# Performance work log

Measured on AMD Instinct MI355X. Metric: run time of the kernel, lower is better.

The kernel has to match this reference:

```python
import jax, jax.numpy as jnp
import numpy as np
from jax import lax

B, T = 256, 256
FD = (768, 74, 35)      # text, audio, vision input feature dims
HD = (128, 64, 64)      # LSTM hidden sizes
LEN = sum(HD)           # 256, fused feature dim
TW = 2                  # time_window
EXT = TW * LEN + 1      # 513, extended_dim
RANK = 24
OUT = 1


def setup_inputs() -> dict:
    key = jax.random.key(0)
    ks = iter(jax.random.split(key, 32))
    def n(shape, scale=0.05):
        return jax.random.normal(next(ks), shape, dtype=jnp.float32) * scale
    inp = {
        "text": n((B, T, FD[0]), 1.0),
        "audio": n((B, T, FD[1]), 1.0),
        "vision": n((B, T, FD[2]), 1.0),
    }
    # LSTM params per subnet: W_ih [4H, D], W_hh [4H, H], combined bias [4H]
    for tag, d, h in (("t", FD[0], HD[0]), ("a", FD[1], HD[1]), ("v", FD[2], HD[2])):
        inp[f"Wih_{tag}"] = n((4 * h, d))
        inp[f"Whh_{tag}"] = n((4 * h, h))
        inp[f"b_{tag}"] = n((4 * h,))
    inp["W1"] = n((RANK * OUT, LEN))
    inp["b1"] = n((RANK * OUT,))
    inp["W2"] = n((RANK * OUT, EXT))
    inp["b2"] = n((RANK * OUT,))
    inp["fw"] = n((1, RANK), 1.0)  # fusion_weights, xavier_normal-like
    return inp


def _lstm_seq(x, Wih, Whh, b):
    # x: [B, T, D] -> all hidden states [B, T, H]; torch gate order i,f,g,o
    Bn = x.shape[0]
    H = Whh.shape[1]
    h0 = jnp.zeros((Bn, H), x.dtype)
    def step(carry, xt):
        h, c = carry
        g = xt @ Wih.T + h @ Whh.T + b
        i, f, gg, o = jnp.split(g, 4, axis=-1)
        c = jax.nn.sigmoid(f) * c + jax.nn.sigmoid(i) * jnp.tanh(gg)
        h = jax.nn.sigmoid(o) * jnp.tanh(c)
        return (h, c), h
    _, hs = lax.scan(step, (h0, h0), jnp.swapaxes(x, 0, 1))
    return jnp.swapaxes(hs, 0, 1)


def reference(text, audio, vision,
              Wih_t, Whh_t, b_t, Wih_a, Whh_a, b_a, Wih_v, Whh_v, b_v,
              W1, b1, W2, b2, fw):
    # SubNets (dropout is identity in eval mode)
    audio_h = _lstm_seq(audio, Wih_a, Whh_a, b_a)
    video_h = _lstm_seq(vision, Wih_v, Whh_v, b_v)
    text_h = _lstm_seq(text, Wih_t, Whh_t, b_t)
    z = jnp.concatenate((audio_h, video_h, text_h), axis=2)  # [B, T, LEN]
    # time_extend with time_window=2: [ones, z[:, i], z[:, (i+1) % T]]
    ones = jnp.ones((z.shape[0], z.shape[1], 1), z.dtype)
    shifts = [jnp.roll(z, -j, axis=1) for j in range(TW)]
    z_ext = jnp.concatenate([ones] + shifts, axis=2)  # [B, T, EXT]
    # fusion loop over idx (stride=1 -> all T), vectorized as batched GEMM + mean
    a = jnp.einsum('btl,rl->btr', z, W1) + b1          # [B, T, RANK*OUT]
    bb = jnp.einsum('bte,re->btr', z_ext, W2) + b2     # [B, T, RANK*OUT]
    z_fusion = (a * bb).mean(axis=1)                   # sum_i/len(idx)
    z_fusion = z_fusion.reshape(-1, RANK, OUT)
    z_output = jnp.einsum('r,bro->bo', fw[0], z_fusion)
    output = z_output.reshape(-1, OUT)
    norm = jnp.sum(jnp.linalg.norm(z.reshape(z.shape[0], -1), axis=1)) / z.shape[0]
    return output, norm
```

## Files before the change

kernel.cpp:

```cpp
#include <hip/hip_runtime.h>
#include <math.h>


typedef unsigned short ushortT;
typedef short bf16x8 __attribute__((ext_vector_type(8)));
typedef float f32x4 __attribute__((ext_vector_type(4)));

__device__ __forceinline__ unsigned int f2bf(float f) {
  unsigned int u = __float_as_uint(f);
  u += 0x7FFFu + ((u >> 16) & 1u);
  return u >> 16;
}
__device__ __forceinline__ unsigned int pk2bf(float lo, float hi) {
  return f2bf(lo) | (f2bf(hi) << 16);
}
__device__ __forceinline__ float bf2f(ushortT u) {
  return __uint_as_float(((unsigned int)u) << 16);
}

template <int KP, int KIN>
__global__ __launch_bounds__(256) void pad_cvt_k(const float* __restrict__ src,
                                                 ushortT* __restrict__ dst, int total) {
  const int i = blockIdx.x * 256 + threadIdx.x;
  if (i >= total) return;
  if constexpr (KP == KIN) {
    dst[i] = (ushortT)f2bf(src[i]);
  } else {
    const int row = i / KP, c = i - row * KP;
    dst[i] = (c < KIN) ? (ushortT)f2bf(src[(size_t)row * KIN + c]) : (ushortT)0;
  }
}

#define SA2 40
__global__ __launch_bounds__(512) void gemm_text2_k(const float* __restrict__ X,
                                                    const ushortT* __restrict__ W16,
                                                    const float* __restrict__ bias,
                                                    ushortT* __restrict__ Y16) {
  const int K = 768, N = 512;
  __shared__ __align__(16) ushortT As[128 * SA2];
  __shared__ __align__(16) ushortT Bs[256 * SA2];
  const unsigned int lin = blockIdx.x;
  const int gb = (int)(lin >> 4), rb = (int)(lin & 15);
  const int m0 = (gb * 8 + (rb & 7)) * 128;
  const int n0 = (rb >> 3) * 256;
  const int tid = threadIdx.x;
  const int wave = tid >> 6, lane = tid & 63;
  const int wr = wave >> 2, wc = wave & 3;
  const int lm = lane & 15, lq = lane >> 4;
  const int arow = tid >> 2, aq = (tid & 3) * 8;
  const int brow = tid >> 1, bq = (tid & 1) * 16;

  const float*   Xp = X + (size_t)(m0 + arow) * K + aq;
  const ushortT* Wp = W16 + (size_t)(n0 + brow) * K + bq;
  uint4* As_w = (uint4*)&As[arow * SA2 + aq];
  uint4* Bs_w = (uint4*)&Bs[brow * SA2 + bq];

  f32x4 acc[4][4];
#pragma unroll
  for (int i = 0; i < 4; i++)
#pragma unroll
    for (int j = 0; j < 4; j++) acc[i][j] = (f32x4){0.f, 0.f, 0.f, 0.f};

  for (int k0 = 0; k0 < K; k0 += 32) {
    const float4 a0 = *(const float4*)(Xp + k0);
    const float4 a1 = *(const float4*)(Xp + k0 + 4);
    const uint4 b0v = *(const uint4*)(Wp + k0);
    const uint4 b1v = *(const uint4*)(Wp + k0 + 8);
    __syncthreads();
    uint4 ao;
    ao.x = pk2bf(a0.x, a0.y); ao.y = pk2bf(a0.z, a0.w);
    ao.z = pk2bf(a1.x, a1.y); ao.w = pk2bf(a1.z, a1.w);
    As_w[0] = ao;
    Bs_w[0] = b0v;
    Bs_w[1] = b1v;
    __syncthreads();
    bf16x8 af[4], bfv[4];
#pragma unroll
    for (int mt = 0; mt < 4; mt++)
      af[mt] = *(const bf16x8*)&As[(wr * 64 + mt * 16 + lm) * SA2 + lq * 8];
#pragma unroll
    for (int nt = 0; nt < 4; nt++)
      bfv[nt] = *(const bf16x8*)&Bs[(wc * 64 + nt * 16 + lm) * SA2 + lq * 8];
#pragma unroll
    for (int mt = 0; mt < 4; mt++)
#pragma unroll
      for (int nt = 0; nt < 4; nt++)
        acc[mt][nt] = __builtin_amdgcn_mfma_f32_16x16x32_bf16(af[mt], bfv[nt], acc[mt][nt], 0, 0, 0);
  }
  float biasv[4];
#pragma unroll
  for (int nt = 0; nt < 4; nt++) biasv[nt] = bias[n0 + wc * 64 + nt * 16 + lm];
#pragma unroll
  for (int mt = 0; mt < 4; mt++) {
#pragma unroll
    for (int nt = 0; nt < 4; nt++) {
      const int row0 = m0 + wr * 64 + mt * 16 + lq * 4;
      const int col = n0 + wc * 64 + nt * 16 + lm;
#pragma unroll
      for (int r = 0; r < 4; r++)
        Y16[(size_t)(row0 + r) * N + col] = (ushortT)f2bf(acc[mt][nt][r] + biasv[nt]);
    }
  }
}

template <int KP>
__global__ __launch_bounds__(256) void gemm_xp_k(const ushortT* __restrict__ A16,
                                                 const ushortT* __restrict__ B16,
                                                 const float* __restrict__ bias,
                                                 ushortT* __restrict__ Y16) {
  constexpr int SB = KP + 8;
  __shared__ __align__(16) ushortT As[128 * SB];
  __shared__ __align__(16) ushortT Bs[128 * SB];
  const int n0 = blockIdx.x * 128;
  const int m0 = blockIdx.y * 128;
  const int tid = threadIdx.x;
  const int srow = tid >> 1, shalf = tid & 1;
  const int wave = tid >> 6, lane = tid & 63;
  const int wr = wave >> 1, wc = wave & 1;
  const int lm = lane & 15, lq = lane >> 4;

  const uint4* ap = (const uint4*)(A16 + (size_t)(m0 + srow) * KP + shalf * (KP / 2));
  const uint4* bp = (const uint4*)(B16 + (size_t)(n0 + srow) * KP + shalf * (KP / 2));
  uint4* aw = (uint4*)&As[srow * SB + shalf * (KP / 2)];
  uint4* bw = (uint4*)&Bs[srow * SB + shalf * (KP / 2)];
#pragma unroll
  for (int i = 0; i < KP / 16; i++) { aw[i] = ap[i]; bw[i] = bp[i]; }
  __syncthreads();

  constexpr int KC = KP / 32;
  f32x4 acc[4][4];
#pragma unroll
  for (int i = 0; i < 4; i++)
#pragma unroll
    for (int j = 0; j < 4; j++) acc[i][j] = (f32x4){0.f, 0.f, 0.f, 0.f};
#pragma unroll
  for (int ks = 0; ks < KC; ks++) {
    bf16x8 af[4], bfv[4];
#pragma unroll
    for (int mt = 0; mt < 4; mt++)
      af[mt] = *(const bf16x8*)&As[(wr * 64 + mt * 16 + lm) * SB + ks * 32 + lq * 8];
#pragma unroll
    for (int nt = 0; nt < 4; nt++)
      bfv[nt] = *(const bf16x8*)&Bs[(wc * 64 + nt * 16 + lm) * SB + ks * 32 + lq * 8];
#pragma unroll
    for (int mt = 0; mt < 4; mt++)
#pragma unroll
      for (int nt = 0; nt < 4; nt++)
        acc[mt][nt] = __builtin_amdgcn_mfma_f32_16x16x32_bf16(af[mt], bfv[nt], acc[mt][nt], 0, 0, 0);
  }
  float biasv[4];
#pragma unroll
  for (int nt = 0; nt < 4; nt++) biasv[nt] = bias[n0 + wc * 64 + nt * 16 + lm];
#pragma unroll
  for (int mt = 0; mt < 4; mt++) {
#pragma unroll
    for (int nt = 0; nt < 4; nt++) {
      const int row0 = m0 + wr * 64 + mt * 16 + lq * 4;
      const int col = n0 + wc * 64 + nt * 16 + lm;
#pragma unroll
      for (int r = 0; r < 4; r++)
        Y16[(size_t)(row0 + r) * 256 + col] = (ushortT)f2bf(acc[mt][nt][r] + biasv[nt]);
    }
  }
}

__device__ __forceinline__ void bar_lgkm() {
  asm volatile("s_waitcnt lgkmcnt(0)" ::: "memory");
  __builtin_amdgcn_sched_barrier(0);
  __builtin_amdgcn_s_barrier();
  __builtin_amdgcn_sched_barrier(0);
}

template <int H, int COFF, int CW>
__device__ __forceinline__ void recur_impl3(const ushortT* __restrict__ xp,
                                            const ushortT* __restrict__ Whh,
                                            ushortT* __restrict__ z,
                                            int bblk, char* smem_) {
  constexpr int KC = H / 32;
  constexpr int C4H = 4 * H;
  constexpr int HP = H + 8;
  constexpr int XP = C4H + 8;
  constexpr int RING = 6;
  constexpr int NCH4 = C4H / 256;
  constexpr int CRB = H / 8;
  constexpr int FPT = (64 * CRB) / 512;
  ushortT* hbuf = (ushortT*)smem_;
  ushortT* xps = hbuf + RING * 16 * HP;
  const int tid = threadIdx.x;
  const int s = tid >> 6, lane = tid & 63;
  const int lm = lane & 15, lq = lane >> 4;
  const int b0 = bblk * 16;
  const int srow = tid >> 5, sch = tid & 31;
  const ushortT* xrowp = xp + (size_t)(b0 + srow) * 256 * C4H + sch * (C4H / 32);
  ushortT* xdst0 = &xps[srow * XP + sch * (C4H / 32)];

  bf16x8 bw[4][KC];
  if (s < CW) {
#pragma unroll
    for (int g = 0; g < 4; g++)
#pragma unroll
      for (int kc = 0; kc < KC; kc++) {
        const int n = g * H + s * 16 + lm;
        bw[g][kc] = *(const bf16x8*)(Whh + (size_t)n * H + kc * 32 + lq * 8);
      }
  }
  for (int i = tid; i < 16 * HP; i += 512) hbuf[(RING - 1) * 16 * HP + i] = 0;

  uint4 svA[NCH4], svB[NCH4];
  {
    const uint4* s0 = (const uint4*)(xrowp);
#pragma unroll
    for (int i = 0; i < NCH4; i++) svA[i] = s0[i];
    uint4* d0 = (uint4*)xdst0;
#pragma unroll
    for (int i = 0; i < NCH4; i++) d0[i] = svA[i];
    const uint4* s1 = (const uint4*)(xrowp + (size_t)C4H);
#pragma unroll
    for (int i = 0; i < NCH4; i++) svB[i] = s1[i];
  }
  float cst[4] = {0.f, 0.f, 0.f, 0.f};
  __syncthreads();

  auto step = [&](int t, uint4 (&svI)[NCH4], uint4 (&svC)[NCH4]) {
    if (t >= 4 && (t & 3) == 0) {
      const int t0 = t - 4;
#pragma unroll
      for (int i = 0; i < FPT; i++) {
        const int q = i * 512 + tid;
        const int m = q / (4 * CRB), j = (q / CRB) & 3, cr = q % CRB;
        const uint4 v = *(const uint4*)&hbuf[((t0 + j) % RING) * 16 * HP + m * HP + cr * 8];
        *(uint4*)&z[((size_t)(b0 + m) * 256 + t0 + j) * 256 + COFF + cr * 8] = v;
      }
    }
    {
      const int tn = (t + 2 < 256) ? t + 2 : 255;
      const uint4* src = (const uint4*)(xrowp + (size_t)tn * C4H);
#pragma unroll
      for (int i = 0; i < NCH4; i++) svI[i] = src[i];
    }
    {
      uint4* dst = (uint4*)(xdst0 + ((t + 1) & 1) * 16 * XP);
#pragma unroll
      for (int i = 0; i < NCH4; i++) dst[i] = svC[i];
    }
    if (s < CW) {
      const ushortT* hb = &hbuf[((t + RING - 1) % RING) * 16 * HP + lm * HP];
      bf16x8 af[KC];
#pragma unroll
      for (int kc = 0; kc < KC; kc++) af[kc] = *(const bf16x8*)(hb + kc * 32 + lq * 8);
      f32x4 acc[4];
#pragma unroll
      for (int g = 0; g < 4; g++) acc[g] = (f32x4){0.f, 0.f, 0.f, 0.f};
#pragma unroll
      for (int kc = 0; kc < KC; kc++)
#pragma unroll
        for (int g = 0; g < 4; g++)
          acc[g] = __builtin_amdgcn_mfma_f32_16x16x32_bf16(af[kc], bw[g][kc], acc[g], 0, 0, 0);
      const ushortT* xb = &xps[(t & 1) * 16 * XP];
      ushortT* hw = &hbuf[(t % RING) * 16 * HP];
      const int col = s * 16 + lm;
#pragma unroll
      for (int r = 0; r < 4; r++) {
        const int xrow = (lq * 4 + r) * XP;
        const float iv = acc[0][r] + bf2f(xb[xrow + 0 * H + col]);
        const float fv = acc[1][r] + bf2f(xb[xrow + 1 * H + col]);
        const float gg = acc[2][r] + bf2f(xb[xrow + 2 * H + col]);
        const float ov = acc[3][r] + bf2f(xb[xrow + 3 * H + col]);
        const float ei = __expf(-iv), ef = __expf(-fv), eg = __expf(-2.f * gg);
        const float pi = 1.f + ei, pf = 1.f + ef, pg = 1.f + eg;
        const float cc = (cst[r] * pi * pg + (1.f - eg) * pf) *
                         __builtin_amdgcn_rcpf(pf * pi * pg);
        cst[r] = cc;
        const float ec = __expf(-2.f * cc), eo = __expf(-ov);
        const float hv = (1.f - ec) * __builtin_amdgcn_rcpf((1.f + eo) * (1.f + ec));
        hw[(lq * 4 + r) * HP + col] = (ushortT)f2bf(hv);
      }
    }
    bar_lgkm();
  };

  for (int t = 0; t < 256; t += 2) {
    step(t, svA, svB);
    step(t + 1, svB, svA);
  }
  {
    const int t0 = 252;
#pragma unroll
    for (int i = 0; i < FPT; i++) {
      const int q = i * 512 + tid;
      const int m = q / (4 * CRB), j = (q / CRB) & 3, cr = q % CRB;
      const uint4 v = *(const uint4*)&hbuf[((t0 + j) % RING) * 16 * HP + m * HP + cr * 8];
      *(uint4*)&z[((size_t)(b0 + m) * 256 + t0 + j) * 256 + COFF + cr * 8] = v;
    }
  }
}

__global__ __launch_bounds__(512, 1) void recur3_k(const ushortT* __restrict__ xpt,
                                                   const ushortT* __restrict__ xpa,
                                                   const ushortT* __restrict__ xpv_,
                                                   const ushortT* __restrict__ Wt,
                                                   const ushortT* __restrict__ Wa,
                                                   const ushortT* __restrict__ Wv,
                                                   ushortT* __restrict__ z) {
  extern __shared__ char smem[];
  const int bid = blockIdx.x;
  if (bid < 16) recur_impl3<128, 128, 8>(xpt, Wt, z, bid, smem);
  else if (bid < 32) recur_impl3<64, 0, 4>(xpa, Wa, z, bid - 16, smem);
  else recur_impl3<64, 64, 4>(xpv_, Wv, z, bid - 32, smem);
}

__global__ __launch_bounds__(192) void fusion_k(const ushortT* __restrict__ z,
                                                const float* __restrict__ W1,
                                                const float* __restrict__ b1,
                                                const float* __restrict__ W2,
                                                const float* __restrict__ b2,
                                                const float* __restrict__ fw,
                                                float* __restrict__ s_acc,
                                                float* __restrict__ sumsq) {
  __shared__ __align__(16) float zs[256 * 36];
  __shared__ float red[8];
  const int tid = threadIdx.x;
  const int b = blockIdx.x >> 3;
  const int t0 = (blockIdx.x & 7) * 32;
  const ushortT* zb = z + (size_t)b * 65536;
  float sq = 0.0f;
  for (int idx = tid; idx < 33 * 256; idx += 192) {
    const int row = idx >> 8, k = idx & 255;
    int t = t0 + row; if (t >= 256) t -= 256;
    const float v = bf2f(zb[t * 256 + k]);
    zs[k * 36 + row] = v;
    if (row < 32) sq += v * v;
  }
  __syncthreads();
  const int dg = tid >> 3;
  const int rg = tid & 7;
  const float* w1p = W1 + dg * 256;
  const float* w2p = W2 + dg * 513;
  float aa[4] = {}, ab1[4] = {}, ab2[4] = {};
#pragma unroll 4
  for (int k = 0; k < 256; k++) {
    const float w1v = w1p[k];
    const float w21 = w2p[1 + k];
    const float w22 = w2p[257 + k];
    const float* zr = &zs[k * 36 + (rg << 2)];
    const float4 za = *(const float4*)zr;
    const float z4 = zr[4];
    aa[0]  += za.x * w1v; aa[1]  += za.y * w1v; aa[2]  += za.z * w1v; aa[3]  += za.w * w1v;
    ab1[0] += za.x * w21; ab1[1] += za.y * w21; ab1[2] += za.z * w21; ab1[3] += za.w * w21;
    ab2[0] += za.y * w22; ab2[1] += za.z * w22; ab2[2] += za.w * w22; ab2[3] += z4   * w22;
  }
  const float b1v = b1[dg];
  const float b2v = b2[dg] + w2p[0];
  const float fwv = fw[dg];
  float s = 0.0f;
#pragma unroll
  for (int i = 0; i < 4; i++) {
    const float a  = aa[i] + b1v;
    const float bb = ab1[i] + ab2[i] + b2v;
    s += a * bb;
  }
  s *= fwv;
#pragma unroll
  for (int off = 32; off > 0; off >>= 1) {
    s  += __shfl_down(s, off);
    sq += __shfl_down(sq, off);
  }
  const int wid = tid >> 6;
  if ((tid & 63) == 0) { red[wid * 2] = s; red[wid * 2 + 1] = sq; }
  __syncthreads();
  if (tid == 0) {
    atomicAdd(&s_acc[b], red[0] + red[2] + red[4]);
    atomicAdd(&sumsq[b], red[1] + red[3] + red[5]);
  }
}

__global__ __launch_bounds__(256) void final_k(const float* __restrict__ s_acc,
                                               const float* __restrict__ sumsq,
                                               float* __restrict__ out) {
  __shared__ float red[4];
  const int tid = threadIdx.x;
  out[tid] = s_acc[tid] * (1.0f / 256.0f);
  float sq = sqrtf(sumsq[tid]);
#pragma unroll
  for (int off = 32; off > 0; off >>= 1) sq += __shfl_down(sq, off);
  if ((tid & 63) == 0) red[tid >> 6] = sq;
  __syncthreads();
  if (tid == 0) out[256] = (red[0] + red[1] + red[2] + red[3]) * (1.0f / 256.0f);
}

extern "C" void kernel_launch(void* const* d_in, const int* in_sizes, int n_in,
                              void* d_out, int out_size, void* d_ws, size_t ws_size,
                              hipStream_t stream) {
  const float* text   = (const float*)d_in[0];
  const float* audio  = (const float*)d_in[1];
  const float* vision = (const float*)d_in[2];
  const float* Wih_t  = (const float*)d_in[3];
  const float* Whh_t  = (const float*)d_in[4];
  const float* b_t    = (const float*)d_in[5];
  const float* Wih_a  = (const float*)d_in[6];
  const float* Whh_a  = (const float*)d_in[7];
  const float* b_a    = (const float*)d_in[8];
  const float* Wih_v  = (const float*)d_in[9];
  const float* Whh_v  = (const float*)d_in[10];
  const float* b_v    = (const float*)d_in[11];
  const float* W1     = (const float*)d_in[12];
  const float* b1     = (const float*)d_in[13];
  const float* W2     = (const float*)d_in[14];
  const float* b2     = (const float*)d_in[15];
  const float* fw     = (const float*)d_in[16];

  ushortT* xpt = (ushortT*)d_ws;
  ushortT* xpa = xpt + (size_t)33554432;
  ushortT* xpv = xpa + (size_t)16777216;
  ushortT* z16 = xpv + (size_t)16777216;
  float* s_acc = (float*)(z16 + (size_t)16777216);
  float* sumsq = s_acc + 256;
  ushortT* WhhT16 = (ushortT*)(sumsq + 256);
  ushortT* WhhA16 = WhhT16 + 65536;
  ushortT* WhhV16 = WhhA16 + 16384;
  ushortT* A16a  = z16;
  ushortT* A16v  = A16a + (size_t)6291456;
  ushortT* Wt768 = A16v + (size_t)4194304;
  ushortT* WA16  = Wt768 + 393216;
  ushortT* WV16  = WA16 + 24576;

  hipMemsetAsync(s_acc, 0, 512 * sizeof(float), stream);

  pad_cvt_k<768, 768><<<1536, 256, 0, stream>>>(Wih_t, Wt768, 512 * 768);
  pad_cvt_k<128, 128><<<256, 256, 0, stream>>>(Whh_t, WhhT16, 512 * 128);
  pad_cvt_k<64, 64><<<64, 256, 0, stream>>>(Whh_a, WhhA16, 256 * 64);
  pad_cvt_k<64, 64><<<64, 256, 0, stream>>>(Whh_v, WhhV16, 256 * 64);
  pad_cvt_k<96, 74><<<96, 256, 0, stream>>>(Wih_a, WA16, 256 * 96);
  pad_cvt_k<64, 35><<<64, 256, 0, stream>>>(Wih_v, WV16, 256 * 64);
  pad_cvt_k<96, 74><<<24576, 256, 0, stream>>>(audio, A16a, 65536 * 96);
  pad_cvt_k<64, 35><<<16384, 256, 0, stream>>>(vision, A16v, 65536 * 64);

  gemm_text2_k<<<1024, 512, 0, stream>>>(text, Wt768, b_t, xpt);
  gemm_xp_k<96><<<dim3(2, 512), 256, 0, stream>>>(A16a, WA16, b_a, xpa);
  gemm_xp_k<64><<<dim3(2, 512), 256, 0, stream>>>(A16v, WV16, b_v, xpv);
  recur3_k<<<48, 512, 59392, stream>>>(xpt, xpa, xpv, WhhT16, WhhA16, WhhV16, z16);
  fusion_k<<<2048, 192, 0, stream>>>(z16, W1, b1, W2, b2, fw, s_acc, sumsq);
  final_k<<<1, 256, 0, stream>>>(s_acc, sumsq, (float*)d_out);
}
```

Measured before the change: 925.4 us.

## Store input projections in per-lane fragment layout so recurrence reads them directly

The input-projection GEMM epilogues now scatter results into a layout ordered by block, timestep and MFMA fragment position. In that layout each compute lane of the recurrence kernel can fetch its gate inputs for a step with two contiguous 16-byte global loads. This drops the previous path that staged projections through shared memory, along with its staging copies and the extra LDS reads per step, and it reduces the dynamic shared memory size. The price is scattered, strided 2-byte global stores in the GEMM epilogues, and the recurrence now depends on global-load latency being hidden by a two-step prefetch.

New measurement: 846.5 us. 8.5% less time.

```diff
diff --git a/kernel.cpp b/kernel.cpp
--- a/kernel.cpp
+++ b/kernel.cpp
@@ -36,7 +36,7 @@
                                                     const ushortT* __restrict__ W16,
                                                     const float* __restrict__ bias,
                                                     ushortT* __restrict__ Y16) {
-  const int K = 768, N = 512;
+  const int K = 768;
   __shared__ __align__(16) ushortT As[128 * SA2];
   __shared__ __align__(16) ushortT Bs[256 * SA2];
   const unsigned int lin = blockIdx.x;
@@ -90,15 +90,23 @@
   float biasv[4];
 #pragma unroll
   for (int nt = 0; nt < 4; nt++) biasv[nt] = bias[n0 + wc * 64 + nt * 16 + lm];
-#pragma unroll
-  for (int mt = 0; mt < 4; mt++) {
-#pragma unroll
-    for (int nt = 0; nt < 4; nt++) {
-      const int row0 = m0 + wr * 64 + mt * 16 + lq * 4;
-      const int col = n0 + wc * 64 + nt * 16 + lm;
+  const int bb = m0 >> 8;
+  const int mq16 = ((bb & 15) >> 2) * 16;
+  const int mr2 = bb & 3;
+  const size_t chunk0 = (size_t)((bb >> 4) * 256) * 8192;
+  const int tbase = (m0 & 255) + wr * 64 + lq * 4;
+#pragma unroll
+  for (int nt = 0; nt < 4; nt++) {
+    const int C = n0 + wc * 64 + nt * 16 + lm;
+    const int g = C >> 7, cc = C & 127;
+    const int off_nt = (g >> 1) * 4096 + ((cc >> 4) * 64 + mq16 + (cc & 15)) * 8 +
+                       (g & 1) * 4 + mr2;
+#pragma unroll
+    for (int mt = 0; mt < 4; mt++) {
+      const size_t a0 = chunk0 + (size_t)(tbase + mt * 16) * 8192 + off_nt;
 #pragma unroll
       for (int r = 0; r < 4; r++)
-        Y16[(size_t)(row0 + r) * N + col] = (ushortT)f2bf(acc[mt][nt][r] + biasv[nt]);
+        Y16[a0 + (size_t)r * 8192] = (ushortT)f2bf(acc[mt][nt][r] + biasv[nt]);
     }
   }
 }
@@ -151,15 +159,23 @@
   float biasv[4];
 #pragma unroll
   for (int nt = 0; nt < 4; nt++) biasv[nt] = bias[n0 + wc * 64 + nt * 16 + lm];
-#pragma unroll
-  for (int mt = 0; mt < 4; mt++) {
-#pragma unroll
-    for (int nt = 0; nt < 4; nt++) {
-      const int row0 = m0 + wr * 64 + mt * 16 + lq * 4;
-      const int col = n0 + wc * 64 + nt * 16 + lm;
+  const int bb = m0 >> 8;
+  const int mq16 = ((bb & 15) >> 2) * 16;
+  const int mr2 = bb & 3;
+  const size_t chunk0 = (size_t)((bb >> 4) * 256) * 4096;
+  const int tbase = (m0 & 255) + wr * 64 + lq * 4;
+#pragma unroll
+  for (int nt = 0; nt < 4; nt++) {
+    const int C = n0 + wc * 64 + nt * 16 + lm;
+    const int g = C >> 6, cc = C & 63;
+    const int off_nt = (g >> 1) * 2048 + ((cc >> 4) * 64 + mq16 + (cc & 15)) * 8 +
+                       (g & 1) * 4 + mr2;
+#pragma unroll
+    for (int mt = 0; mt < 4; mt++) {
+      const size_t a0 = chunk0 + (size_t)(tbase + mt * 16) * 4096 + off_nt;
 #pragma unroll
       for (int r = 0; r < 4; r++)
-        Y16[(size_t)(row0 + r) * 256 + col] = (ushortT)f2bf(acc[mt][nt][r] + biasv[nt]);
+        Y16[a0 + (size_t)r * 4096] = (ushortT)f2bf(acc[mt][nt][r] + biasv[nt]);
     }
   }
 }
@@ -172,30 +188,26 @@
 }
 
 template <int H, int COFF, int CW>
-__device__ __forceinline__ void recur_impl3(const ushortT* __restrict__ xp,
+__device__ __forceinline__ void recur_impl4(const ushortT* __restrict__ xp,
                                             const ushortT* __restrict__ Whh,
                                             ushortT* __restrict__ z,
                                             int bblk, char* smem_) {
   constexpr int KC = H / 32;
-  constexpr int C4H = 4 * H;
   constexpr int HP = H + 8;
-  constexpr int XP = C4H + 8;
   constexpr int RING = 6;
-  constexpr int NCH4 = C4H / 256;
   constexpr int CRB = H / 8;
   constexpr int FPT = (64 * CRB) / 512;
+  constexpr int TS = CW * 64 * 16;
   ushortT* hbuf = (ushortT*)smem_;
-  ushortT* xps = hbuf + RING * 16 * HP;
   const int tid = threadIdx.x;
   const int s = tid >> 6, lane = tid & 63;
   const int lm = lane & 15, lq = lane >> 4;
   const int b0 = bblk * 16;
-  const int srow = tid >> 5, sch = tid & 31;
-  const ushortT* xrowp = xp + (size_t)(b0 + srow) * 256 * C4H + sch * (C4H / 32);
-  ushortT* xdst0 = &xps[srow * XP + sch * (C4H / 32)];
+  const bool comp = (s < CW);
+  const ushortT* xg = xp + (size_t)(bblk * 256) * TS + tid * 8;
 
   bf16x8 bw[4][KC];
-  if (s < CW) {
+  if (comp) {
 #pragma unroll
     for (int g = 0; g < 4; g++)
 #pragma unroll
@@ -206,22 +218,17 @@
   }
   for (int i = tid; i < 16 * HP; i += 512) hbuf[(RING - 1) * 16 * HP + i] = 0;
 
-  uint4 svA[NCH4], svB[NCH4];
-  {
-    const uint4* s0 = (const uint4*)(xrowp);
-#pragma unroll
-    for (int i = 0; i < NCH4; i++) svA[i] = s0[i];
-    uint4* d0 = (uint4*)xdst0;
-#pragma unroll
-    for (int i = 0; i < NCH4; i++) d0[i] = svA[i];
-    const uint4* s1 = (const uint4*)(xrowp + (size_t)C4H);
-#pragma unroll
-    for (int i = 0; i < NCH4; i++) svB[i] = s1[i];
+  uint4 gA[2], gB[2];
+  if (comp) {
+    gA[0] = *(const uint4*)(xg);
+    gA[1] = *(const uint4*)(xg + TS / 2);
+    gB[0] = *(const uint4*)(xg + TS);
+    gB[1] = *(const uint4*)(xg + TS + TS / 2);
   }
   float cst[4] = {0.f, 0.f, 0.f, 0.f};
   __syncthreads();
 
-  auto step = [&](int t, uint4 (&svI)[NCH4], uint4 (&svC)[NCH4]) {
+  auto step = [&](int t, uint4 (&gCur)[2]) {
     if (t >= 4 && (t & 3) == 0) {
       const int t0 = t - 4;
 #pragma unroll
@@ -232,18 +239,20 @@
         *(uint4*)&z[((size_t)(b0 + m) * 256 + t0 + j) * 256 + COFF + cr * 8] = v;
       }
     }
-    {
+    if (comp) {
+      unsigned int w[8] = {gCur[0].x, gCur[0].y, gCur[0].z, gCur[0].w,
+                           gCur[1].x, gCur[1].y, gCur[1].z, gCur[1].w};
+      float ad[4][4];
+#pragma unroll
+      for (int g = 0; g < 4; g++)
+#pragma unroll
+        for (int r = 0; r < 4; r++) {
+          const unsigned int ww = w[g * 2 + (r >> 1)];
+          ad[g][r] = __uint_as_float((r & 1) ? (ww & 0xffff0000u) : (ww << 16));
+        }
       const int tn = (t + 2 < 256) ? t + 2 : 255;
-      const uint4* src = (const uint4*)(xrowp + (size_t)tn * C4H);
-#pragma unroll
-      for (int i = 0; i < NCH4; i++) svI[i] = src[i];
-    }
-    {
-      uint4* dst = (uint4*)(xdst0 + ((t + 1) & 1) * 16 * XP);
-#pragma unroll
-      for (int i = 0; i < NCH4; i++) dst[i] = svC[i];
-    }
-    if (s < CW) {
+      gCur[0] = *(const uint4*)(xg + (size_t)tn * TS);
+      gCur[1] = *(const uint4*)(xg + (size_t)tn * TS + TS / 2);
       const ushortT* hb = &hbuf[((t + RING - 1) % RING) * 16 * HP + lm * HP];
       bf16x8 af[KC];
 #pragma unroll
@@ -256,16 +265,14 @@
 #pragma unroll
         for (int g = 0; g < 4; g++)
           acc[g] = __builtin_amdgcn_mfma_f32_16x16x32_bf16(af[kc], bw[g][kc], acc[g], 0, 0, 0);
-      const ushortT* xb = &xps[(t & 1) * 16 * XP];
       ushortT* hw = &hbuf[(t % RING) * 16 * HP];
       const int col = s * 16 + lm;
 #pragma unroll
       for (int r = 0; r < 4; r++) {
-        const int xrow = (lq * 4 + r) * XP;
-        const float iv = acc[0][r] + bf2f(xb[xrow + 0 * H + col]);
-        const float fv = acc[1][r] + bf2f(xb[xrow + 1 * H + col]);
-        const float gg = acc[2][r] + bf2f(xb[xrow + 2 * H + col]);
-        const float ov = acc[3][r] + bf2f(xb[xrow + 3 * H + col]);
+        const float iv = acc[0][r] + ad[0][r];
+        const float fv = acc[1][r] + ad[1][r];
+        const float gg = acc[2][r] + ad[2][r];
+        const float ov = acc[3][r] + ad[3][r];
         const float ei = __expf(-iv), ef = __expf(-fv), eg = __expf(-2.f * gg);
         const float pi = 1.f + ei, pf = 1.f + ef, pg = 1.f + eg;
         const float cc = (cst[r] * pi * pg + (1.f - eg) * pf) *
@@ -280,8 +287,8 @@
   };
 
   for (int t = 0; t < 256; t += 2) {
-    step(t, svA, svB);
-    step(t + 1, svB, svA);
+    step(t, gA);
+    step(t + 1, gB);
   }
   {
     const int t0 = 252;
@@ -295,7 +302,7 @@
   }
 }
 
-__global__ __launch_bounds__(512, 1) void recur3_k(const ushortT* __restrict__ xpt,
+__global__ __launch_bounds__(512, 1) void recur4_k(const ushortT* __restrict__ xpt,
                                                    const ushortT* __restrict__ xpa,
                                                    const ushortT* __restrict__ xpv_,
                                                    const ushortT* __restrict__ Wt,
@@ -304,9 +311,9 @@
                                                    ushortT* __restrict__ z) {
   extern __shared__ char smem[];
   const int bid = blockIdx.x;
-  if (bid < 16) recur_impl3<128, 128, 8>(xpt, Wt, z, bid, smem);
-  else if (bid < 32) recur_impl3<64, 0, 4>(xpa, Wa, z, bid - 16, smem);
-  else recur_impl3<64, 64, 4>(xpv_, Wv, z, bid - 32, smem);
+  if (bid < 16) recur_impl4<128, 128, 8>(xpt, Wt, z, bid, smem);
+  else if (bid < 32) recur_impl4<64, 0, 4>(xpa, Wa, z, bid - 16, smem);
+  else recur_impl4<64, 64, 4>(xpv_, Wv, z, bid - 32, smem);
 }
 
 __global__ __launch_bounds__(192) void fusion_k(const ushortT* __restrict__ z,
@@ -438,7 +445,7 @@
   gemm_text2_k<<<1024, 512, 0, stream>>>(text, Wt768, b_t, xpt);
   gemm_xp_k<96><<<dim3(2, 512), 256, 0, stream>>>(A16a, WA16, b_a, xpa);
   gemm_xp_k<64><<<dim3(2, 512), 256, 0, stream>>>(A16v, WV16, b_v, xpv);
-  recur3_k<<<48, 512, 59392, stream>>>(xpt, xpa, xpv, WhhT16, WhhA16, WhhV16, z16);
+  recur4_k<<<48, 512, 26112, stream>>>(xpt, xpa, xpv, WhhT16, WhhA16, WhhV16, z16);
   fusion_k<<<2048, 192, 0, stream>>>(z16, W1, b1, W2, b2, fw, s_acc, sumsq);
   final_k<<<1, 256, 0, stream>>>(s_acc, sumsq, (float*)d_out);
 }
```
